# Kernel tuning notes

Hardware: AMD Instinct MI355X
Metric: run time of the kernel (lower is better)

Reference implementation:

```python
import jax, jax.numpy as jnp
import numpy as np

D_MODEL = 2048
NUM_HEADS = 16
HEAD_DIM = 128
ROPE_BASE = 10000.0
NEG_INF = -1e9


def setup_inputs() -> dict:
    key = jax.random.key(0)
    ks = jax.random.split(key, 5)
    B, S = 2, 2048
    hidden_states = jax.random.normal(ks[0], (B, S, D_MODEL), dtype=jnp.float32)
    # additive causal mask: 0 on/below diagonal, large-negative above
    causal = jnp.triu(jnp.full((S, S), NEG_INF, dtype=jnp.float32), k=1)
    attention_mask = jnp.broadcast_to(causal, (B, 1, S, S))
    position_ids = jnp.broadcast_to(jnp.arange(S, dtype=jnp.int32), (B, S))
    scale = 1.0 / np.sqrt(D_MODEL)
    Wq = jax.random.normal(ks[1], (D_MODEL, NUM_HEADS * HEAD_DIM), dtype=jnp.float32) * scale
    Wk = jax.random.normal(ks[2], (D_MODEL, NUM_HEADS * HEAD_DIM), dtype=jnp.float32) * scale
    Wv = jax.random.normal(ks[3], (D_MODEL, NUM_HEADS * HEAD_DIM), dtype=jnp.float32) * scale
    Wo = jax.random.normal(ks[4], (NUM_HEADS * HEAD_DIM, D_MODEL), dtype=jnp.float32) * scale
    return {"hidden_states": hidden_states, "attention_mask": attention_mask,
            "position_ids": position_ids, "Wq": Wq, "Wk": Wk, "Wv": Wv, "Wo": Wo}


def _rope_cos_sin(position_ids):
    # inv_freq: [head_dim/2]
    inv_freq = 1.0 / (ROPE_BASE ** (jnp.arange(0, HEAD_DIM, 2, dtype=jnp.float32) / HEAD_DIM))
    freqs = position_ids.astype(jnp.float32)[..., None] * inv_freq  # [B,S,hd/2]
    emb = jnp.concatenate([freqs, freqs], axis=-1)  # [B,S,hd]
    return jnp.cos(emb), jnp.sin(emb)


def _rotate_half(x):
    x1, x2 = jnp.split(x, 2, axis=-1)
    return jnp.concatenate([-x2, x1], axis=-1)


def reference(hidden_states, attention_mask, position_ids, Wq, Wk, Wv, Wo):
    B, S, _ = hidden_states.shape
    H, Dh = NUM_HEADS, HEAD_DIM
    q = (hidden_states @ Wq).reshape(B, S, H, Dh).transpose(0, 2, 1, 3)  # [B,H,S,Dh]
    k = (hidden_states @ Wk).reshape(B, S, H, Dh).transpose(0, 2, 1, 3)
    v = (hidden_states @ Wv).reshape(B, S, H, Dh).transpose(0, 2, 1, 3)
    cos, sin = _rope_cos_sin(position_ids)  # [B,S,Dh]
    cos = cos[:, None, :, :]  # [B,1,S,Dh]
    sin = sin[:, None, :, :]
    q = q * cos + _rotate_half(q) * sin
    k = k * cos + _rotate_half(k) * sin
    scaling = 1.0 / np.sqrt(Dh)
    scores = jnp.einsum('bhqd,bhkd->bhqk', q, k) * scaling  # [B,H,S,S]
    scores = scores + attention_mask[:, :, :, :S]
    attn = jax.nn.softmax(scores.astype(jnp.float32), axis=-1).astype(q.dtype)
    # dropout p=0.0 / eval mode -> identity
    out = jnp.einsum('bhqk,bhkd->bhqd', attn, v)  # [B,H,S,Dh]
    out = out.transpose(0, 2, 1, 3).reshape(B, S, H * Dh)
    return out @ Wo
```

## Files before the change

### kernel.cpp

```cpp
#include <hip/hip_runtime.h>

typedef __attribute__((ext_vector_type(4))) float f32x4;
typedef __attribute__((ext_vector_type(8))) _Float16 f16x8;
typedef __attribute__((ext_vector_type(4))) _Float16 f16x4;

#define SEQ 2048
#define DM 2048
#define NQKV 6144

__device__ __forceinline__ void gload16(const _Float16* g, _Float16* l) {
  __builtin_amdgcn_global_load_lds(
      (const __attribute__((address_space(1))) void*)g,
      (__attribute__((address_space(3))) void*)l, 16, 0, 0);
}

__global__ __launch_bounds__(256) void cvt_x_kernel(const float* __restrict__ X,
                                                    _Float16* __restrict__ Xb, int n4) {
  int i = blockIdx.x * 256 + threadIdx.x;
  if (i < n4) {
    const float4 v = ((const float4*)X)[i];
    f16x4 o;
    o.x = (_Float16)v.x; o.y = (_Float16)v.y; o.z = (_Float16)v.z; o.w = (_Float16)v.w;
    ((f16x4*)Xb)[i] = o;
  }
}

__global__ __launch_bounds__(256) void wtrans_all_kernel(const float* __restrict__ Wq,
                                                         const float* __restrict__ Wk,
                                                         const float* __restrict__ Wv,
                                                         const float* __restrict__ Wo,
                                                         _Float16* __restrict__ Wqkvt,
                                                         _Float16* __restrict__ Wot) {
  __shared__ float tile[32][33];
  const int z = blockIdx.z;
  const float* W = (z == 0) ? Wq : (z == 1) ? Wk : (z == 2) ? Wv : Wo;
  _Float16* Wt = (z < 3) ? (Wqkvt + (size_t)z * 2048 * 2048) : Wot;
  const int n0 = blockIdx.x * 32, k0 = blockIdx.y * 32;
  const int tx = threadIdx.x & 31, ty = threadIdx.x >> 5;
#pragma unroll
  for (int i = 0; i < 32; i += 8)
    tile[ty + i][tx] = W[(size_t)(k0 + ty + i) * 2048 + n0 + tx];
  __syncthreads();
#pragma unroll
  for (int i = 0; i < 32; i += 8)
    Wt[(size_t)(n0 + ty + i) * 2048 + k0 + tx] = (_Float16)tile[tx][ty + i];
}

__global__ __launch_bounds__(256) void rope_table_kernel(float* __restrict__ ct,
                                                         float* __restrict__ st) {
  int i = blockIdx.x * 256 + threadIdx.x;
  int pos = i >> 6, f = i & 63;
  float inv = powf(10000.0f, -(float)f / 64.0f);
  float ang = (float)pos * inv;
  ct[i] = cosf(ang);
  st[i] = sinf(ang);
}

template <bool OUTF32>
__global__ __launch_bounds__(512, 2) void gemm8_kernel(const _Float16* __restrict__ A,
                                                       const _Float16* __restrict__ Bt,
                                                       void* __restrict__ Cout,
                                                       int M, int N, int K) {
  __shared__ __align__(16) _Float16 As[2 * 16384];
  __shared__ __align__(16) _Float16 Bs[2 * 16384];
  const int nwg = gridDim.x * gridDim.y;
  const int orig = blockIdx.y * gridDim.x + blockIdx.x;
  const int id = (orig & 7) * (nwg >> 3) + (orig >> 3);
  const int bx = id % gridDim.x, by = id / gridDim.x;
  const int bm = by * 256, bn = bx * 256;
  const int t = threadIdx.x, lane = t & 63, w = t >> 6;
  const int wm = w >> 2, wn = w & 3;
  const int rl = lane & 15, lr4 = lane >> 4;
  const int NKT = K >> 6;

  const int srow = t >> 3;
  const int scol = ((t & 7) ^ (srow & 7)) << 3;
  const _Float16* pA = A + (size_t)(bm + srow) * K + scol;
  const _Float16* pB = Bt + (size_t)(bn + srow) * K + scol;
  _Float16* lA = As + t * 8;
  _Float16* lB = Bs + t * 8;
  const size_t rowK64 = (size_t)64 * K;

#define STAGE_A(h, kt)                                                                     \
  { const int _b = (kt) & 1; const size_t _g = (size_t)((h) * 128) * K + (size_t)(kt) * 64; \
    gload16(pA + _g, lA + _b * 16384 + (h) * 8192);                                        \
    gload16(pA + _g + rowK64, lA + _b * 16384 + (h) * 8192 + 4096); }
#define STAGE_B(h, kt)                                                                     \
  { const int _b = (kt) & 1; const size_t _g = (size_t)((h) * 128) * K + (size_t)(kt) * 64; \
    gload16(pB + _g, lB + _b * 16384 + (h) * 8192);                                        \
    gload16(pB + _g + rowK64, lB + _b * 16384 + (h) * 8192 + 4096); }

  const int sw0 = (lr4 ^ (rl & 7)) << 3;
  const int sw1 = ((4 + lr4) ^ (rl & 7)) << 3;
  const int aoff = (wm * 64 + rl) * 64;
  const int boff = (wn * 32 + rl) * 64;

  f16x8 a_[4][2], b0_[2][2], b1_[2][2];
  f32x4 acc[2][2][4][2];
#pragma unroll
  for (int qm = 0; qm < 2; ++qm)
#pragma unroll
    for (int qn = 0; qn < 2; ++qn)
#pragma unroll
      for (int mf = 0; mf < 4; ++mf)
#pragma unroll
        for (int nf = 0; nf < 2; ++nf) acc[qm][qn][mf][nf] = (f32x4)0.0f;

#define LOAD_A(QM, BUF)                                                 \
  { const _Float16* _p = As + (BUF) * 16384 + (QM) * 8192 + aoff;       \
    _Pragma("unroll") for (int mf = 0; mf < 4; ++mf) {                  \
      a_[mf][0] = *(const f16x8*)&_p[mf * 1024 + sw0];                  \
      a_[mf][1] = *(const f16x8*)&_p[mf * 1024 + sw1]; } }
#define LOAD_B(DST, QN, BUF)                                            \
  { const _Float16* _p = Bs + (BUF) * 16384 + (QN) * 8192 + boff;       \
    _Pragma("unroll") for (int nf = 0; nf < 2; ++nf) {                  \
      DST[nf][0] = *(const f16x8*)&_p[nf * 1024 + sw0];                 \
      DST[nf][1] = *(const f16x8*)&_p[nf * 1024 + sw1]; } }
#define MFMA_Q(QM, QN, BREG)                                            \
  __builtin_amdgcn_s_setprio(1);                                        \
  _Pragma("unroll") for (int mf = 0; mf < 4; ++mf)                      \
    _Pragma("unroll") for (int nf = 0; nf < 2; ++nf) {                  \
      acc[QM][QN][mf][nf] = __builtin_amdgcn_mfma_f32_16x16x32_f16(     \
          a_[mf][0], BREG[nf][0], acc[QM][QN][mf][nf], 0, 0, 0);        \
      acc[QM][QN][mf][nf] = __builtin_amdgcn_mfma_f32_16x16x32_f16(     \
          a_[mf][1], BREG[nf][1], acc[QM][QN][mf][nf], 0, 0, 0); }      \
  __builtin_amdgcn_s_setprio(0);
#define BAR()                                                           \
  do { __builtin_amdgcn_sched_barrier(0); __builtin_amdgcn_s_barrier(); \
       __builtin_amdgcn_sched_barrier(0); } while (0)
#define LGKM0()                                                         \
  do { asm volatile("s_waitcnt lgkmcnt(0)" ::: "memory");               \
       __builtin_amdgcn_sched_barrier(0); } while (0)

  STAGE_A(0, 0); STAGE_B(0, 0); STAGE_A(1, 0); STAGE_B(1, 0);
  STAGE_A(0, 1); STAGE_B(0, 1);
  asm volatile("s_waitcnt vmcnt(4)" ::: "memory");
  BAR();

  for (int j = 0; j < NKT; ++j) {
    const int buf = j & 1;
    LOAD_A(0, buf); LOAD_B(b0_, 0, buf);
    if (j + 1 < NKT) STAGE_A(1, j + 1);
    BAR(); LGKM0();
    MFMA_Q(0, 0, b0_);
    BAR();
    LOAD_B(b1_, 1, buf);
    if (j + 1 < NKT) STAGE_B(1, j + 1);
    BAR(); LGKM0();
    MFMA_Q(0, 1, b1_);
    BAR();
    LOAD_A(1, buf);
    if (j + 2 < NKT) STAGE_A(0, j + 2);
    BAR(); LGKM0();
    MFMA_Q(1, 0, b0_);
    BAR();
    if (j + 2 < NKT) STAGE_B(0, j + 2);
    BAR(); LGKM0();
    MFMA_Q(1, 1, b1_);
    if (j < NKT - 2)       { asm volatile("s_waitcnt vmcnt(4)" ::: "memory"); }
    else if (j == NKT - 2) { asm volatile("s_waitcnt vmcnt(0)" ::: "memory"); }
    BAR();
  }

#pragma unroll
  for (int qm = 0; qm < 2; ++qm)
#pragma unroll
    for (int qn = 0; qn < 2; ++qn)
#pragma unroll
      for (int mf = 0; mf < 4; ++mf)
#pragma unroll
        for (int nf = 0; nf < 2; ++nf) {
          const int col = bn + qn * 128 + wn * 32 + nf * 16 + rl;
#pragma unroll
          for (int ri = 0; ri < 4; ++ri) {
            const int row = bm + qm * 128 + wm * 64 + mf * 16 + lr4 * 4 + ri;
            if (OUTF32)
              ((float*)Cout)[(size_t)row * N + col] = acc[qm][qn][mf][nf][ri];
            else
              ((_Float16*)Cout)[(size_t)row * N + col] = (_Float16)acc[qm][qn][mf][nf][ri];
          }
        }
#undef STAGE_A
#undef STAGE_B
#undef LOAD_A
#undef LOAD_B
#undef MFMA_Q
#undef BAR
#undef LGKM0
}

template <bool OUTF32>
__global__ __launch_bounds__(256) void gemm3_kernel(const _Float16* __restrict__ A,
                                                    const _Float16* __restrict__ Bt,
                                                    void* __restrict__ Cout,
                                                    int M, int N, int K) {
  __shared__ __align__(16) _Float16 As[128 * 64];
  __shared__ __align__(16) _Float16 Bs[128 * 64];
  const int nwg = gridDim.x * gridDim.y;
  const int orig = blockIdx.y * gridDim.x + blockIdx.x;
  const int id = (orig & 7) * (nwg >> 3) + (orig >> 3);
  const int bx = id % gridDim.x, by = id / gridDim.x;
  const int bm = by * 128, bn = bx * 128;
  const int t = threadIdx.x, lane = t & 63;
  const int w = t >> 6, wm = w >> 1, wn = w & 1;
  const int rl = lane & 15, lr4 = lane >> 4;

  f32x4 acc[4][4];
#pragma unroll
  for (int i = 0; i < 4; ++i)
#pragma unroll
    for (int j = 0; j < 4; ++j) acc[i][j] = (f32x4)0.0f;

  for (int kt = 0; kt < K; kt += 64) {
#pragma unroll
    for (int i = 0; i < 4; ++i) {
      const int c = i * 256 + t;
      const int row = c >> 3, u = c & 7;
      gload16(&A[(size_t)(bm + row) * K + kt + ((u ^ (row & 7)) << 3)], &As[c * 8]);
    }
#pragma unroll
    for (int i = 0; i < 4; ++i) {
      const int c = i * 256 + t;
      const int row = c >> 3, u = c & 7;
      gload16(&Bt[(size_t)(bn + row) * K + kt + ((u ^ (row & 7)) << 3)], &Bs[c * 8]);
    }
    __syncthreads();
#pragma unroll
    for (int kk = 0; kk < 2; ++kk) {
      f16x8 af[4], bf[4];
#pragma unroll
      for (int i = 0; i < 4; ++i) {
        const int row = wm * 64 + i * 16 + rl;
        af[i] = *(const f16x8*)&As[row * 64 + (((kk * 4 + lr4) ^ (row & 7)) << 3)];
      }
#pragma unroll
      for (int j = 0; j < 4; ++j) {
        const int row = wn * 64 + j * 16 + rl;
        bf[j] = *(const f16x8*)&Bs[row * 64 + (((kk * 4 + lr4) ^ (row & 7)) << 3)];
      }
#pragma unroll
      for (int i = 0; i < 4; ++i)
#pragma unroll
        for (int j = 0; j < 4; ++j)
          acc[i][j] = __builtin_amdgcn_mfma_f32_16x16x32_f16(af[i], bf[j], acc[i][j], 0, 0, 0);
    }
    __syncthreads();
  }
#pragma unroll
  for (int i = 0; i < 4; ++i)
#pragma unroll
    for (int j = 0; j < 4; ++j) {
      const int col = bn + wn * 64 + j * 16 + rl;
#pragma unroll
      for (int ri = 0; ri < 4; ++ri) {
        const int row = bm + wm * 64 + i * 16 + lr4 * 4 + ri;
        if (OUTF32)
          ((float*)Cout)[(size_t)row * N + col] = acc[i][j][ri];
        else
          ((_Float16*)Cout)[(size_t)row * N + col] = (_Float16)acc[i][j][ri];
      }
    }
}

__global__ __launch_bounds__(256) void rope_qk_kernel(const _Float16* __restrict__ QKVo,
                                                      const int* __restrict__ pos_ids,
                                                      const float* __restrict__ ct,
                                                      const float* __restrict__ st,
                                                      _Float16* __restrict__ Q,
                                                      _Float16* __restrict__ K) {
  int id = blockIdx.x * 256 + threadIdx.x;
  int f = id & 63;
  int h = (id >> 6) & 15;
  int s_ = (id >> 10) & 2047;
  int b = (id >> 21) & 1;
  int row = b * SEQ + s_;
  int pos = pos_ids[row];
  float c = ct[pos * 64 + f], sn = st[pos * 64 + f];
  size_t base = (size_t)row * NQKV;
  float q1 = (float)QKVo[base + h * 128 + f];
  float q2 = (float)QKVo[base + h * 128 + f + 64];
  float k1 = (float)QKVo[base + 2048 + h * 128 + f];
  float k2 = (float)QKVo[base + 2048 + h * 128 + f + 64];
  const float scale = 0.08838834764831845f;
  size_t obase = (((size_t)(b * 16 + h)) * SEQ + s_) * 128;
  Q[obase + f]      = (_Float16)((q1 * c - q2 * sn) * scale);
  Q[obase + f + 64] = (_Float16)((q2 * c + q1 * sn) * scale);
  K[obase + f]      = (_Float16)(k1 * c - k2 * sn);
  K[obase + f + 64] = (_Float16)(k2 * c + k1 * sn);
}

__global__ __launch_bounds__(256) void v_transpose_kernel(const _Float16* __restrict__ QKVo,
                                                          _Float16* __restrict__ Vt) {
  __shared__ _Float16 tile[32][40];
  const int s0 = blockIdx.x * 32, d0 = blockIdx.y * 32, bh = blockIdx.z;
  const int b = bh >> 4, h = bh & 15;
  const int tx = threadIdx.x & 31, ty = threadIdx.x >> 5;
#pragma unroll
  for (int i = 0; i < 32; i += 8) {
    int s_ = s0 + ty + i;
    tile[ty + i][tx] = QKVo[(size_t)(b * SEQ + s_) * NQKV + 4096 + h * 128 + d0 + tx];
  }
  __syncthreads();
#pragma unroll
  for (int i = 0; i < 32; i += 8) {
    int d = d0 + ty + i;
    Vt[((size_t)bh * 128 + d) * SEQ + s0 + tx] = tile[tx][ty + i];
  }
}

__global__ __launch_bounds__(512) void attn_kernel(const _Float16* __restrict__ Q,
                                                   const _Float16* __restrict__ K,
                                                   const _Float16* __restrict__ Vt,
                                                   _Float16* __restrict__ O) {
  __shared__ __align__(16) _Float16 Ks[2][64 * 128];
  __shared__ __align__(16) _Float16 Vs[2][128 * 64];
  __shared__ __align__(16) _Float16 Ps[8][16 * 72];
  const int bh = blockIdx.x;
  const int pair = blockIdx.y;
  const int b = bh >> 4, h = bh & 15;
  const int t = threadIdx.x, lane = t & 63, w = t >> 6;
  const int lr = lane >> 4, lc = lane & 15;
  const _Float16* Qb = Q + (size_t)bh * SEQ * 128;
  const _Float16* Kb = K + (size_t)bh * SEQ * 128;
  const _Float16* Vb = Vt + (size_t)bh * 128 * SEQ;

  auto stage = [&](int buf, int kb) {
    const int k0 = kb * 64;
#pragma unroll
    for (int i = 0; i < 2; ++i) {
      const int c = i * 512 + t;
      const int row = c >> 4, u = c & 15;
      gload16(&Kb[(size_t)(k0 + row) * 128 + ((u ^ (row & 7)) * 8)], &Ks[buf][c * 8]);
    }
#pragma unroll
    for (int i = 0; i < 2; ++i) {
      const int c = i * 512 + t;
      const int dim = c >> 3, u = c & 7;
      gload16(&Vb[(size_t)dim * SEQ + k0 + ((u ^ (dim & 7)) * 8)], &Vs[buf][c * 8]);
    }
  };

  for (int half = 0; half < 2; ++half) {
    const int j = half ? (15 - pair) : pair;
    const int q0 = j * 128;
    const int nkb = 2 * j + 2;
    const int rowmin = q0 + w * 16;

    f16x8 qf[4];
    {
      const int qrow = q0 + w * 16 + lc;
#pragma unroll
      for (int kk = 0; kk < 4; ++kk)
        qf[kk] = *(const f16x8*)&Qb[(size_t)qrow * 128 + kk * 32 + lr * 8];
    }
    f32x4 acco[8];
#pragma unroll
    for (int i = 0; i < 8; ++i) acco[i] = (f32x4)0.0f;
    float m_r[4] = {-1e30f, -1e30f, -1e30f, -1e30f};
    float l_r[4] = {0.f, 0.f, 0.f, 0.f};

    stage(0, 0);
    __syncthreads();
    for (int kb = 0; kb < nkb; ++kb) {
      const int cur = kb & 1;
      if (kb + 1 < nkb) stage(cur ^ 1, kb + 1);
      const int k0 = kb * 64;
      if (k0 <= rowmin + 15) {
        f32x4 sacc[4];
#pragma unroll
        for (int jj = 0; jj < 4; ++jj) sacc[jj] = (f32x4)0.0f;
#pragma unroll
        for (int jj = 0; jj < 4; ++jj) {
          const int krow = jj * 16 + lc;
#pragma unroll
          for (int kk = 0; kk < 4; ++kk) {
            const int idx = (krow * 128 + kk * 32 + lr * 8) ^ ((krow & 7) << 3);
            f16x8 kf = *(const f16x8*)&Ks[cur][idx];
            sacc[jj] = __builtin_amdgcn_mfma_f32_16x16x32_f16(qf[kk], kf, sacc[jj], 0, 0, 0);
          }
        }
        const bool diag = (k0 + 63 > rowmin);
#pragma unroll
        for (int r = 0; r < 4; ++r) {
          const int rowi = rowmin + lr * 4 + r;
          float s[4], mx = -1e30f;
#pragma unroll
          for (int jj = 0; jj < 4; ++jj) {
            float sv = sacc[jj][r];
            if (diag && (k0 + jj * 16 + lc > rowi)) sv = -1e30f;
            s[jj] = sv;
            mx = fmaxf(mx, sv);
          }
#pragma unroll
          for (int msk = 1; msk < 16; msk <<= 1) mx = fmaxf(mx, __shfl_xor(mx, msk));
          const float mn = fmaxf(m_r[r], mx);
          const float sc = __expf(m_r[r] - mn);
          float rs = 0.f;
#pragma unroll
          for (int jj = 0; jj < 4; ++jj) {
            float pv = __expf(s[jj] - mn);
            rs += pv;
            Ps[w][(lr * 4 + r) * 72 + jj * 16 + lc] = (_Float16)pv;
          }
#pragma unroll
          for (int msk = 1; msk < 16; msk <<= 1) rs += __shfl_xor(rs, msk);
          l_r[r] = l_r[r] * sc + rs;
          m_r[r] = mn;
#pragma unroll
          for (int tt = 0; tt < 8; ++tt) acco[tt][r] *= sc;
        }
#pragma unroll
        for (int tt = 0; tt < 8; ++tt) {
          const int dim = tt * 16 + lc;
#pragma unroll
          for (int ch = 0; ch < 2; ++ch) {
            f16x8 pf = *(const f16x8*)&Ps[w][lc * 72 + ch * 32 + lr * 8];
            const int vidx = (dim * 64 + ch * 32 + lr * 8) ^ ((dim & 7) << 3);
            f16x8 vf = *(const f16x8*)&Vs[cur][vidx];
            acco[tt] = __builtin_amdgcn_mfma_f32_16x16x32_f16(pf, vf, acco[tt], 0, 0, 0);
          }
        }
      }
      __syncthreads();
    }
#pragma unroll
    for (int tt = 0; tt < 8; ++tt) {
      const int col = h * 128 + tt * 16 + lc;
#pragma unroll
      for (int r = 0; r < 4; ++r) {
        const int row = q0 + w * 16 + lr * 4 + r;
        O[(size_t)(b * SEQ + row) * DM + col] = (_Float16)(acco[tt][r] / l_r[r]);
      }
    }
  }
}

extern "C" void kernel_launch(void* const* d_in, const int* in_sizes, int n_in,
                              void* d_out, int out_size, void* d_ws, size_t ws_size,
                              hipStream_t stream) {
  const float* hidden = (const float*)d_in[0];
  const int* pos_ids = (const int*)d_in[2];
  const float* Wq = (const float*)d_in[3];
  const float* Wk = (const float*)d_in[4];
  const float* Wv = (const float*)d_in[5];
  const float* Wo = (const float*)d_in[6];

  char* ws = (char*)d_ws;
  _Float16* Xb    = (_Float16*)(ws + 0);
  _Float16* Wqkvt = (_Float16*)(ws + 16777216);
  _Float16* Wot   = (_Float16*)(ws + 41943040);
  _Float16* QKVo  = (_Float16*)(ws + 50331648);
  _Float16* Kbuf  = (_Float16*)(ws + 100663296);
  float* ct       = (float*)(ws + 117440512);
  float* st       = (float*)(ws + 117964800);
  _Float16* Vtbuf = Xb;
  _Float16* Qbuf  = Wqkvt;
  _Float16* Obuf  = QKVo;

  cvt_x_kernel<<<8192, 256, 0, stream>>>(hidden, Xb, 2097152);
  wtrans_all_kernel<<<dim3(64, 64, 4), 256, 0, stream>>>(Wq, Wk, Wv, Wo, Wqkvt, Wot);
  rope_table_kernel<<<512, 256, 0, stream>>>(ct, st);

  gemm8_kernel<false><<<dim3(24, 16), 512, 0, stream>>>(Xb, Wqkvt, QKVo, 4096, 6144, 2048);

  rope_qk_kernel<<<16384, 256, 0, stream>>>(QKVo, pos_ids, ct, st, Qbuf, Kbuf);
  v_transpose_kernel<<<dim3(64, 4, 32), 256, 0, stream>>>(QKVo, Vtbuf);

  attn_kernel<<<dim3(32, 8), 512, 0, stream>>>(Qbuf, Kbuf, Vtbuf, Obuf);

  gemm3_kernel<true><<<dim3(16, 32), 256, 0, stream>>>(Obuf, Wot, d_out, 4096, 2048, 2048);
}
```

Before: 303.8 us.

## Restructure 256x256 GEMM main loop into two-tile unrolled pipeline with deeper prefetch

Rewrites the double-buffered K loop of the 256x256 GEMM kernel so each iteration handles two k-tiles, with the LDS buffer index fixed at compile time. Global-to-LDS stages are issued earlier, and the next tile's first B fragment is read from LDS right after the last MFMA quadrant. One barrier-separated phase is folded away. The goal is to keep more loads in flight (vmcnt 6 instead of 4) and cut barrier and waiting overhead between MFMA phases. The cost is a longer, hand-scheduled sequence whose buffer-reuse hazards are subtle, and it assumes NKT is even.

```diff
diff --git a/kernel.cpp b/kernel.cpp
--- a/kernel.cpp
+++ b/kernel.cpp
@@ -81,14 +81,14 @@
   _Float16* lB = Bs + t * 8;
   const size_t rowK64 = (size_t)64 * K;
 
-#define STAGE_A(h, kt)                                                                     \
-  { const int _b = (kt) & 1; const size_t _g = (size_t)((h) * 128) * K + (size_t)(kt) * 64; \
-    gload16(pA + _g, lA + _b * 16384 + (h) * 8192);                                        \
-    gload16(pA + _g + rowK64, lA + _b * 16384 + (h) * 8192 + 4096); }
-#define STAGE_B(h, kt)                                                                     \
-  { const int _b = (kt) & 1; const size_t _g = (size_t)((h) * 128) * K + (size_t)(kt) * 64; \
-    gload16(pB + _g, lB + _b * 16384 + (h) * 8192);                                        \
-    gload16(pB + _g + rowK64, lB + _b * 16384 + (h) * 8192 + 4096); }
+#define STA(H, KT, BUF)                                                   \
+  { const size_t _g = (size_t)((H) * 128) * K + (size_t)(KT) * 64;        \
+    gload16(pA + _g, lA + (BUF) * 16384 + (H) * 8192);                    \
+    gload16(pA + _g + rowK64, lA + (BUF) * 16384 + (H) * 8192 + 4096); }
+#define STB(H, KT, BUF)                                                   \
+  { const size_t _g = (size_t)((H) * 128) * K + (size_t)(KT) * 64;        \
+    gload16(pB + _g, lB + (BUF) * 16384 + (H) * 8192);                    \
+    gload16(pB + _g + rowK64, lB + (BUF) * 16384 + (H) * 8192 + 4096); }
 
   const int sw0 = (lr4 ^ (rl & 7)) << 3;
   const int sw1 = ((4 + lr4) ^ (rl & 7)) << 3;
@@ -132,34 +132,59 @@
   do { asm volatile("s_waitcnt lgkmcnt(0)" ::: "memory");               \
        __builtin_amdgcn_sched_barrier(0); } while (0)
 
-  STAGE_A(0, 0); STAGE_B(0, 0); STAGE_A(1, 0); STAGE_B(1, 0);
-  STAGE_A(0, 1); STAGE_B(0, 1);
-  asm volatile("s_waitcnt vmcnt(4)" ::: "memory");
+  STA(0, 0, 0); STB(0, 0, 0); STA(1, 0, 0); STB(1, 0, 0);
+  STA(0, 1, 1); STB(0, 1, 1); STA(1, 1, 1);
+  asm volatile("s_waitcnt vmcnt(6)" ::: "memory");
   BAR();
-
-  for (int j = 0; j < NKT; ++j) {
-    const int buf = j & 1;
-    LOAD_A(0, buf); LOAD_B(b0_, 0, buf);
-    if (j + 1 < NKT) STAGE_A(1, j + 1);
-    BAR(); LGKM0();
-    MFMA_Q(0, 0, b0_);
-    BAR();
-    LOAD_B(b1_, 1, buf);
-    if (j + 1 < NKT) STAGE_B(1, j + 1);
-    BAR(); LGKM0();
-    MFMA_Q(0, 1, b1_);
-    BAR();
-    LOAD_A(1, buf);
-    if (j + 2 < NKT) STAGE_A(0, j + 2);
-    BAR(); LGKM0();
-    MFMA_Q(1, 0, b0_);
-    BAR();
-    if (j + 2 < NKT) STAGE_B(0, j + 2);
-    BAR(); LGKM0();
+  LOAD_B(b0_, 0, 0);
+
+  for (int i = 0; i < (NKT >> 1) - 1; ++i) {
+    const int k1 = 2 * i + 1, k2 = 2 * i + 2, k3 = 2 * i + 3;
+    LOAD_A(0, 0); STB(1, k1, 1);
+    BAR(); LGKM0(); MFMA_Q(0, 0, b0_); BAR();
+    LOAD_B(b1_, 1, 0); STA(0, k2, 0);
+    BAR(); LGKM0(); MFMA_Q(0, 1, b1_); BAR();
+    LOAD_A(1, 0); STB(0, k2, 0);
+    BAR(); LGKM0(); MFMA_Q(1, 0, b0_); BAR();
+    STA(1, k2, 0);
+    asm volatile("s_waitcnt vmcnt(6)" ::: "memory");
+    BAR();
     MFMA_Q(1, 1, b1_);
-    if (j < NKT - 2)       { asm volatile("s_waitcnt vmcnt(4)" ::: "memory"); }
-    else if (j == NKT - 2) { asm volatile("s_waitcnt vmcnt(0)" ::: "memory"); }
-    BAR();
+    LOAD_B(b0_, 0, 1);
+    BAR();
+    LOAD_A(0, 1); STB(1, k2, 0);
+    BAR(); LGKM0(); MFMA_Q(0, 0, b0_); BAR();
+    LOAD_B(b1_, 1, 1); STA(0, k3, 1);
+    BAR(); LGKM0(); MFMA_Q(0, 1, b1_); BAR();
+    LOAD_A(1, 1); STB(0, k3, 1);
+    BAR(); LGKM0(); MFMA_Q(1, 0, b0_); BAR();
+    STA(1, k3, 1);
+    asm volatile("s_waitcnt vmcnt(6)" ::: "memory");
+    BAR();
+    MFMA_Q(1, 1, b1_);
+    LOAD_B(b0_, 0, 0);
+    BAR();
+  }
+  {
+    const int k1 = NKT - 1;
+    LOAD_A(0, 0); STB(1, k1, 1);
+    BAR(); LGKM0(); MFMA_Q(0, 0, b0_); BAR();
+    LOAD_B(b1_, 1, 0);
+    BAR(); LGKM0(); MFMA_Q(0, 1, b1_); BAR();
+    LOAD_A(1, 0);
+    BAR(); LGKM0(); MFMA_Q(1, 0, b0_); BAR();
+    asm volatile("s_waitcnt vmcnt(0)" ::: "memory");
+    BAR();
+    MFMA_Q(1, 1, b1_);
+    LOAD_B(b0_, 0, 1);
+    BAR();
+    LOAD_A(0, 1);
+    BAR(); LGKM0(); MFMA_Q(0, 0, b0_); BAR();
+    LOAD_B(b1_, 1, 1);
+    BAR(); LGKM0(); MFMA_Q(0, 1, b1_); BAR();
+    LOAD_A(1, 1);
+    BAR(); LGKM0(); MFMA_Q(1, 0, b0_); BAR();
+    MFMA_Q(1, 1, b1_);
   }
 
 #pragma unroll
@@ -180,8 +205,8 @@
               ((_Float16*)Cout)[(size_t)row * N + col] = (_Float16)acc[qm][qn][mf][nf][ri];
           }
         }
-#undef STAGE_A
-#undef STAGE_B
+#undef STA
+#undef STB
 #undef LOAD_A
 #undef LOAD_B
 #undef MFMA_Q
```

New measurement: 298.2 us. Within noise of the previous version (-1.8%).
